# Optimization experiments

Measured on AMD Instinct MI355X. Metric: run time of the kernel, lower is better.

The kernel has to match this reference:

```python
import jax, jax.numpy as jnp
import numpy as np
from jax.ops import segment_sum

N = 100000
E = 3200000
IN_DIM = 128
HID = 64
L = 3
BN_EPS = 1e-5

def setup_inputs() -> dict:
    key = jax.random.key(0)
    ks = jax.random.split(key, 20)
    s = lambda k, *shape: jax.random.normal(k, shape, dtype=jnp.float32) * 0.05
    inp = {
        'x': jax.random.normal(ks[0], (N, IN_DIM), dtype=jnp.float32),
        'edge_index': jax.random.randint(ks[1], (2, E), 0, N, dtype=jnp.int32),
        'W_in': s(ks[2], IN_DIM, HID), 'b_in': jnp.zeros((HID,), jnp.float32),
        'W_gcn': s(ks[3], L, HID, HID), 'b_gcn': jnp.zeros((L, HID), jnp.float32),
        'bn_gamma': jnp.ones((L, HID), jnp.float32), 'bn_beta': jnp.zeros((L, HID), jnp.float32),
        'W_s1': s(ks[4], 3, HID // 2), 'b_s1': jnp.zeros((HID // 2,), jnp.float32),
        'W_s2': s(ks[5], HID // 2, HID), 'b_s2': jnp.zeros((HID,), jnp.float32),
        'W_o1': s(ks[6], 2 * HID, HID), 'b_o1': jnp.zeros((HID,), jnp.float32),
        'W_o2': s(ks[7], HID, HID // 2), 'b_o2': jnp.zeros((HID // 2,), jnp.float32),
        'W_o3': s(ks[8], HID // 2, 1), 'b_o3': jnp.zeros((1,), jnp.float32),
    }
    return inp

def _gcn_norm(row, col, n):
    # add self-loops, symmetric normalization (PyG GCNConv default)
    loop = jnp.arange(n, dtype=row.dtype)
    row_sl = jnp.concatenate([row, loop])
    col_sl = jnp.concatenate([col, loop])
    deg = segment_sum(jnp.ones_like(col_sl, jnp.float32), col_sl, num_segments=n)
    dis = jnp.where(deg > 0, jax.lax.rsqrt(jnp.maximum(deg, 1.0)), 0.0)
    norm = dis[row_sl] * dis[col_sl]
    return row_sl, col_sl, norm

def _structural(row, col, n):
    # vectorized equivalent of the O(N*E) python loops
    ones = jnp.ones(row.shape[0], jnp.float32)
    deg = segment_sum(ones, row, num_segments=n)          # out-degree over edge_index[0]
    dmax = deg.max()
    norm_deg = jnp.where(dmax > 0, deg / dmax, deg)
    infl_sum = segment_sum(deg[col], row, num_segments=n)  # sum of neighbor degrees
    infl = jnp.where(deg > 0, infl_sum / jnp.maximum(deg, 1.0), 0.0)
    imax = infl.max()
    infl = jnp.where(imax > 0, infl / imax, infl)
    clustering = jnp.zeros(n, jnp.float32)
    return jnp.stack([norm_deg, clustering, infl], axis=1)  # [N,3]

def reference(x, edge_index, W_in, b_in, W_gcn, b_gcn, bn_gamma, bn_beta,
              W_s1, b_s1, W_s2, b_s2, W_o1, b_o1, W_o2, b_o2, W_o3, b_o3):
    n = x.shape[0]
    row, col = edge_index[0], edge_index[1]
    h = x @ W_in + b_in
    row_sl, col_sl, norm = _gcn_norm(row, col, n)
    bn_scale = bn_gamma / jnp.sqrt(1.0 + BN_EPS)  # eval BN: running_mean=0, running_var=1
    for i in range(L):
        hw = h @ W_gcn[i]
        msg = hw[row_sl] * norm[:, None]              # [E+N, HID]
        h = segment_sum(msg, col_sl, num_segments=n) + b_gcn[i]
        h = h * bn_scale[i] + bn_beta[i]
        h = jax.nn.relu(h)
    sf = _structural(row, col, n)
    se = jax.nn.relu(sf @ W_s1 + b_s1) @ W_s2 + b_s2
    h = jnp.concatenate([h, se], axis=1)              # [N, 2*HID]
    h = jax.nn.relu(h @ W_o1 + b_o1)
    h = jax.nn.relu(h @ W_o2 + b_o2)
    return jax.nn.sigmoid(h @ W_o3 + b_o3)            # [N, 1]
```

## Files before the change

kernel.cpp:

```cpp
#include <hip/hip_runtime.h>
#include <hip/hip_bf16.h>
#include <hip/hip_fp16.h>

#define NBU8 65536
#define NB16 32768
#define TPBH 1024

__global__ void k_init(unsigned* __restrict__ maxima) {
    if (threadIdx.x < 2) maxima[threadIdx.x] = 0u;
}

__global__ __launch_bounds__(TPBH) void kh_hist(const int* __restrict__ keys,
                                                unsigned char* __restrict__ part,
                                                int E, int chunk, int npu) {
    __shared__ unsigned bins[NBU8 / 4];
    int b = blockIdx.x, t = threadIdx.x;
    int base = blockIdx.y * NBU8;
    int e0 = b * chunk, e1 = min(E, e0 + chunk);
    for (int j = t; j < NBU8 / 4; j += TPBH) bins[j] = 0u;
    __syncthreads();
    for (int e = e0 + t; e < e1; e += TPBH) {
        int k = keys[e] - base;
        if ((unsigned)k < NBU8) atomicAdd(&bins[k >> 2], 1u << ((k & 3) << 3));
    }
    __syncthreads();
    unsigned* dst = (unsigned*)(part + (size_t)b * npu + base);
    for (int j = t; j < NBU8 / 4; j += TPBH) dst[j] = bins[j];
}

__global__ __launch_bounds__(256) void k_scan1(const unsigned char* __restrict__ part,
                                               int nb, int npu,
                                               int* __restrict__ cnt,
                                               int* __restrict__ roff,
                                               int* __restrict__ bsum, int n) {
    __shared__ int s[256];
    int b = blockIdx.x, t = threadIdx.x;
    int i = b * 256 + t;
    int v = 0;
    if (i < n) {
        for (int k = 0; k < nb; ++k) v += part[(size_t)k * npu + i];
        cnt[i] = v;
    }
    s[t] = v;
    __syncthreads();
    for (int off = 1; off < 256; off <<= 1) {
        int x = (t >= off) ? s[t - off] : 0;
        __syncthreads();
        s[t] += x;
        __syncthreads();
    }
    if (i < n) roff[i] = s[t] - v;
    if (t == 255) bsum[b] = s[255];
}

__global__ __launch_bounds__(512) void k_scan2(int* __restrict__ bsum, int nb) {
    __shared__ int s[512];
    int t = threadIdx.x;
    int v = (t < nb) ? bsum[t] : 0;
    s[t] = v;
    __syncthreads();
    for (int off = 1; off < 512; off <<= 1) {
        int x = (t >= off) ? s[t - off] : 0;
        __syncthreads();
        s[t] += x;
        __syncthreads();
    }
    if (t < nb) bsum[t] = s[t] - v;
}

__global__ void k_scan3(int* __restrict__ roff, const int* __restrict__ bsum,
                        const int* __restrict__ cnt, float* __restrict__ dis, int n, int E) {
    int i = blockIdx.x * blockDim.x + threadIdx.x;
    if (i < n) {
        roff[i] += bsum[i >> 8];
        dis[i] = rsqrtf((float)cnt[i] + 1.0f);
    }
    if (i == 0) roff[n] = E;
}

__global__ void kh_prefix(unsigned char* __restrict__ part, int nb, int npu, int n) {
    int i = blockIdx.x * blockDim.x + threadIdx.x;
    if (i >= n) return;
    int run = 0;
    for (int g = 0; g < 8; ++g) {
        for (int b = g; b < nb; b += 8) {
            size_t idx = (size_t)b * npu + i;
            int v = part[idx];
            part[idx] = (unsigned char)run;
            run += v;
        }
    }
}

__global__ __launch_bounds__(TPBH) void kh_fill(const int* __restrict__ col,
                                                const int* __restrict__ row,
                                                const int* __restrict__ roff,
                                                const unsigned char* __restrict__ pref,
                                                int* __restrict__ esrc,
                                                int E, int chunk, int npu) {
    __shared__ unsigned curs[NBU8 / 4];
    int b = blockIdx.x, t = threadIdx.x;
    int base = blockIdx.y * NBU8;
    int e0 = b * chunk, e1 = min(E, e0 + chunk);
    for (int j = t; j < NBU8 / 4; j += TPBH) curs[j] = 0u;
    __syncthreads();
    const unsigned char* pb = pref + (size_t)b * npu;
    for (int e = e0 + t; e < e1; e += TPBH) {
        int c = col[e], r = row[e];
        int cl = c - base;
        if ((unsigned)cl < NBU8) {
            unsigned sh = (cl & 3) << 3;
            unsigned old = atomicAdd(&curs[cl >> 2], 1u << sh);
            unsigned local = (old >> sh) & 0xFFu;
            int slot = roff[c] + (int)pb[c] + (int)local;
            esrc[slot] = r;
        }
    }
}

__global__ __launch_bounds__(TPBH) void kh_histacc(const int* __restrict__ row,
                                                   const int* __restrict__ col,
                                                   const int* __restrict__ odeg_i,
                                                   unsigned short* __restrict__ part,
                                                   int E, int chunk, int npu) {
    __shared__ unsigned bins[NB16 / 2];
    int b = blockIdx.x, t = threadIdx.x;
    int base = blockIdx.y * NB16;
    int e0 = b * chunk, e1 = min(E, e0 + chunk);
    for (int j = t; j < NB16 / 2; j += TPBH) bins[j] = 0u;
    __syncthreads();
    for (int e = e0 + t; e < e1; e += TPBH) {
        int r = row[e] - base;
        if ((unsigned)r < NB16)
            atomicAdd(&bins[r >> 1], (unsigned)odeg_i[col[e]] << ((r & 1) << 4));
    }
    __syncthreads();
    unsigned* dst = (unsigned*)(part + (size_t)b * npu + base);
    for (int j = t; j < NB16 / 2; j += TPBH) dst[j] = bins[j];
}

__global__ void kh_reduce_odeg(const unsigned char* __restrict__ part,
                               float* __restrict__ odeg, int* __restrict__ odeg_i,
                               unsigned* __restrict__ maxima, int nb, int npu, int n) {
    int i = blockIdx.x * blockDim.x + threadIdx.x;
    float od = 0.f;
    if (i < n) {
        int s = 0;
        for (int b = 0; b < nb; ++b) s += part[(size_t)b * npu + i];
        od = (float)s;
        odeg[i] = od;
        odeg_i[i] = s;
    }
    for (int off = 32; off > 0; off >>= 1) od = fmaxf(od, __shfl_down(od, off));
    if ((threadIdx.x & 63) == 0) atomicMax(&maxima[0], __float_as_uint(od));
}

__global__ void kh_reduce_infl(const unsigned short* __restrict__ part,
                               const float* __restrict__ odeg,
                               float* __restrict__ infl, unsigned* __restrict__ maxima,
                               int nb, int npu, int n) {
    int i = blockIdx.x * blockDim.x + threadIdx.x;
    float fin = 0.f;
    if (i < n) {
        int s = 0;
        for (int b = 0; b < nb; ++b) s += part[(size_t)b * npu + i];
        float od = odeg[i];
        fin = (od > 0.f) ? (float)s / od : 0.f;
        infl[i] = fin;
    }
    for (int off = 32; off > 0; off >>= 1) fin = fmaxf(fin, __shfl_down(fin, off));
    if ((threadIdx.x & 63) == 0) atomicMax(&maxima[1], __float_as_uint(fin));
}

__global__ __launch_bounds__(256) void k_in_proj(const float* __restrict__ x,
                                                 const float* __restrict__ W,
                                                 const float* __restrict__ b,
                                                 float* __restrict__ h, int n) {
    __shared__ alignas(16) float Ws[128 * 64];
    __shared__ alignas(16) float xs[64 * 64];
    int t = threadIdx.x;
    int r0 = blockIdx.x * 64;
    for (int i = t; i < 128 * 64; i += 256) Ws[i] = W[i];

    int c = t & 63, rg = t >> 6;
    float acc[16];
    float bc = b[c];
#pragma unroll
    for (int i = 0; i < 16; ++i) acc[i] = bc;

    const float4* xs4 = (const float4*)xs;
    for (int half = 0; half < 2; ++half) {
        __syncthreads();
        for (int i = t; i < 64 * 16; i += 256) {
            int rr = i >> 4, k4 = i & 15;
            int r = r0 + rr;
            float4 v = (r < n) ? ((const float4*)x)[(size_t)r * 32 + half * 16 + k4]
                               : make_float4(0.f, 0.f, 0.f, 0.f);
            ((float4*)xs)[i] = v;
        }
        __syncthreads();
        for (int k4 = 0; k4 < 16; ++k4) {
            int kk = half * 64 + k4 * 4;
            float w0 = Ws[(kk + 0) * 64 + c];
            float w1 = Ws[(kk + 1) * 64 + c];
            float w2 = Ws[(kk + 2) * 64 + c];
            float w3 = Ws[(kk + 3) * 64 + c];
#pragma unroll
            for (int i = 0; i < 16; ++i) {
                float4 xv = xs4[(rg * 16 + i) * 16 + k4];
                acc[i] = fmaf(xv.x, w0, fmaf(xv.y, w1, fmaf(xv.z, w2, fmaf(xv.w, w3, acc[i]))));
            }
        }
    }
#pragma unroll
    for (int i = 0; i < 16; ++i) {
        int r = r0 + rg * 16 + i;
        if (r < n) h[(size_t)r * 64 + c] = acc[i];
    }
}

__global__ __launch_bounds__(256) void k_gcn_mm(const float* __restrict__ h,
                                                const float* __restrict__ Wg,
                                                const float* __restrict__ dis,
                                                unsigned* __restrict__ hws, int n) {
    __shared__ alignas(16) float Ws[64 * 64];
    __shared__ alignas(16) float xs[64 * 64];
    int t = threadIdx.x;
    int r0 = blockIdx.x * 64;
    for (int i = t; i < 64 * 64; i += 256) Ws[i] = Wg[i];
    for (int i = t; i < 64 * 16; i += 256) {
        int rr = i >> 4, k4 = i & 15;
        int r = r0 + rr;
        float4 v = (r < n) ? ((const float4*)h)[(size_t)r * 16 + k4]
                           : make_float4(0.f, 0.f, 0.f, 0.f);
        ((float4*)xs)[i] = v;
    }
    __syncthreads();
    int c2 = (t & 31) << 1, rg = t >> 5;
    const float4* xs4 = (const float4*)xs;
    float a0[8], a1[8];
#pragma unroll
    for (int i = 0; i < 8; ++i) { a0[i] = 0.f; a1[i] = 0.f; }
    for (int k4 = 0; k4 < 16; ++k4) {
        float wA0 = Ws[(k4 * 4 + 0) * 64 + c2],     wB0 = Ws[(k4 * 4 + 0) * 64 + c2 + 1];
        float wA1 = Ws[(k4 * 4 + 1) * 64 + c2],     wB1 = Ws[(k4 * 4 + 1) * 64 + c2 + 1];
        float wA2 = Ws[(k4 * 4 + 2) * 64 + c2],     wB2 = Ws[(k4 * 4 + 2) * 64 + c2 + 1];
        float wA3 = Ws[(k4 * 4 + 3) * 64 + c2],     wB3 = Ws[(k4 * 4 + 3) * 64 + c2 + 1];
#pragma unroll
        for (int i = 0; i < 8; ++i) {
            float4 xv = xs4[(rg * 8 + i) * 16 + k4];
            a0[i] = fmaf(xv.x, wA0, fmaf(xv.y, wA1, fmaf(xv.z, wA2, fmaf(xv.w, wA3, a0[i]))));
            a1[i] = fmaf(xv.x, wB0, fmaf(xv.y, wB1, fmaf(xv.z, wB2, fmaf(xv.w, wB3, a1[i]))));
        }
    }
#pragma unroll
    for (int i = 0; i < 8; ++i) {
        int r = r0 + rg * 8 + i;
        if (r < n) {
            float d = dis[r];
            __half2 hv = __floats2half2_rn(a0[i] * d, a1[i] * d);
            hws[(size_t)r * 32 + (t & 31)] = *(unsigned*)&hv;
        }
    }
}

__global__ __launch_bounds__(256) void k_gather(const int* __restrict__ roff,
                                                const int* __restrict__ esrc,
                                                const uint2* __restrict__ hws,
                                                const float* __restrict__ dis,
                                                const float* __restrict__ bg,
                                                const float* __restrict__ gamma,
                                                const float* __restrict__ beta,
                                                float* __restrict__ h, int n) {
    int t = threadIdx.x;
    int node = blockIdx.x * 16 + (t >> 4);
    int fl = t & 15;
    if (node >= n) return;

    int beg = roff[node], end = roff[node + 1];
    float acc0 = 0.f, acc1 = 0.f, acc2 = 0.f, acc3 = 0.f;
    union { unsigned u; __half2 h2; } cv;
#define ACC(a) { cv.u = (a).x; float2 f = __half22float2(cv.h2); acc0 += f.x; acc1 += f.y; \
                 cv.u = (a).y; f = __half22float2(cv.h2);        acc2 += f.x; acc3 += f.y; }
    {
        uint2 a = hws[(size_t)node * 16 + fl];
        ACC(a)
    }
    int e = beg;
    for (; e + 4 <= end; e += 4) {
        int r0 = esrc[e], r1 = esrc[e + 1], r2 = esrc[e + 2], r3 = esrc[e + 3];
        uint2 a = hws[(size_t)r0 * 16 + fl];
        uint2 b = hws[(size_t)r1 * 16 + fl];
        uint2 c = hws[(size_t)r2 * 16 + fl];
        uint2 d = hws[(size_t)r3 * 16 + fl];
        ACC(a) ACC(b) ACC(c) ACC(d)
    }
    for (; e < end; ++e) {
        uint2 a = hws[(size_t)esrc[e] * 16 + fl];
        ACC(a)
    }
#undef ACC
    float d = dis[node];
    float inv = rsqrtf(1.0f + 1e-5f);
    float4 g4 = ((const float4*)gamma)[fl];
    float4 b4 = ((const float4*)beta)[fl];
    float4 bg4 = ((const float4*)bg)[fl];
    float4 o;
    o.x = fmaxf(fmaf(acc0 * d + bg4.x, g4.x * inv, b4.x), 0.0f);
    o.y = fmaxf(fmaf(acc1 * d + bg4.y, g4.y * inv, b4.y), 0.0f);
    o.z = fmaxf(fmaf(acc2 * d + bg4.z, g4.z * inv, b4.z), 0.0f);
    o.w = fmaxf(fmaf(acc3 * d + bg4.w, g4.w * inv, b4.w), 0.0f);
    ((float4*)h)[(size_t)node * 16 + fl] = o;
}

__global__ __launch_bounds__(256) void k_final(const float* __restrict__ h,
                                               const float* __restrict__ odeg,
                                               const float* __restrict__ infl,
                                               const unsigned* __restrict__ maxima,
                                               const float* __restrict__ Ws1, const float* __restrict__ bs1,
                                               const float* __restrict__ Ws2, const float* __restrict__ bs2,
                                               const float* __restrict__ Wo1, const float* __restrict__ bo1,
                                               const float* __restrict__ Wo2, const float* __restrict__ bo2,
                                               const float* __restrict__ Wo3, const float* __restrict__ bo3,
                                               float* __restrict__ out, int n) {
    __shared__ alignas(16) float sWs1[96], sbs1[32], sWs2T[64 * 32], sbs2[64];
    __shared__ alignas(16) float sWo1[128 * 64], sbo1[64], sWo2[64 * 32], sbo2[32], sWo3[32];
    int t = threadIdx.x;
    for (int i = t; i < 96; i += 256) sWs1[i] = Ws1[i];
    for (int i = t; i < 2048; i += 256) {
        int j = i >> 6, k = i & 63;
        sWs2T[k * 32 + j] = Ws2[i];
    }
    for (int i = t; i < 8192; i += 256) sWo1[i] = Wo1[i];
    for (int i = t; i < 2048; i += 256) sWo2[i] = Wo2[i];
    if (t < 32) { sbs1[t] = bs1[t]; sbo2[t] = bo2[t]; sWo3[t] = Wo3[t]; }
    if (t < 64) { sbs2[t] = bs2[t]; sbo1[t] = bo1[t]; }
    __syncthreads();

    int i = blockIdx.x * 256 + t;
    if (i >= n) return;

    float dmax = __uint_as_float(maxima[0]);
    float imax = __uint_as_float(maxima[1]);
    float od = odeg[i];
    float sf0 = (dmax > 0.0f) ? od / dmax : od;
    float fin = infl[i];
    float sf2 = (imax > 0.0f) ? fin / imax : fin;

    float hid[32];
#pragma unroll
    for (int j = 0; j < 32; ++j)
        hid[j] = fmaxf(fmaf(sf0, sWs1[j], fmaf(sf2, sWs1[64 + j], sbs1[j])), 0.0f);

    float o1[64];
    const float4* sbo1_4 = (const float4*)sbo1;
#pragma unroll
    for (int c4 = 0; c4 < 16; ++c4) {
        float4 v = sbo1_4[c4];
        o1[c4 * 4] = v.x; o1[c4 * 4 + 1] = v.y; o1[c4 * 4 + 2] = v.z; o1[c4 * 4 + 3] = v.w;
    }

    const float4* sWo1_4 = (const float4*)sWo1;
    const float4* hrow = (const float4*)(h + (size_t)i * 64);
    for (int k4 = 0; k4 < 16; ++k4) {
        float4 hv = hrow[k4];
        float hv_[4] = {hv.x, hv.y, hv.z, hv.w};
#pragma unroll
        for (int j = 0; j < 4; ++j) {
            float hk = hv_[j];
            int k = k4 * 4 + j;
#pragma unroll
            for (int c4 = 0; c4 < 16; ++c4) {
                float4 w = sWo1_4[k * 16 + c4];
                o1[c4 * 4]     = fmaf(hk, w.x, o1[c4 * 4]);
                o1[c4 * 4 + 1] = fmaf(hk, w.y, o1[c4 * 4 + 1]);
                o1[c4 * 4 + 2] = fmaf(hk, w.z, o1[c4 * 4 + 2]);
                o1[c4 * 4 + 3] = fmaf(hk, w.w, o1[c4 * 4 + 3]);
            }
        }
    }
    const float4* sWs2T_4 = (const float4*)sWs2T;
    for (int k = 0; k < 64; ++k) {
        float sek = sbs2[k];
#pragma unroll
        for (int j4 = 0; j4 < 8; ++j4) {
            float4 w = sWs2T_4[k * 8 + j4];
            sek = fmaf(hid[j4 * 4], w.x, fmaf(hid[j4 * 4 + 1], w.y,
                  fmaf(hid[j4 * 4 + 2], w.z, fmaf(hid[j4 * 4 + 3], w.w, sek))));
        }
#pragma unroll
        for (int c4 = 0; c4 < 16; ++c4) {
            float4 w = sWo1_4[(64 + k) * 16 + c4];
            o1[c4 * 4]     = fmaf(sek, w.x, o1[c4 * 4]);
            o1[c4 * 4 + 1] = fmaf(sek, w.y, o1[c4 * 4 + 1]);
            o1[c4 * 4 + 2] = fmaf(sek, w.z, o1[c4 * 4 + 2]);
            o1[c4 * 4 + 3] = fmaf(sek, w.w, o1[c4 * 4 + 3]);
        }
    }

    float o2[32];
    const float4* sbo2_4 = (const float4*)sbo2;
#pragma unroll
    for (int c4 = 0; c4 < 8; ++c4) {
        float4 v = sbo2_4[c4];
        o2[c4 * 4] = v.x; o2[c4 * 4 + 1] = v.y; o2[c4 * 4 + 2] = v.z; o2[c4 * 4 + 3] = v.w;
    }
    const float4* sWo2_4 = (const float4*)sWo2;
#pragma unroll
    for (int c = 0; c < 64; ++c) {
        float v = fmaxf(o1[c], 0.0f);
#pragma unroll
        for (int c4 = 0; c4 < 8; ++c4) {
            float4 w = sWo2_4[c * 8 + c4];
            o2[c4 * 4]     = fmaf(v, w.x, o2[c4 * 4]);
            o2[c4 * 4 + 1] = fmaf(v, w.y, o2[c4 * 4 + 1]);
            o2[c4 * 4 + 2] = fmaf(v, w.z, o2[c4 * 4 + 2]);
            o2[c4 * 4 + 3] = fmaf(v, w.w, o2[c4 * 4 + 3]);
        }
    }

    float o3 = bo3[0];
#pragma unroll
    for (int c2 = 0; c2 < 32; ++c2)
        o3 = fmaf(fmaxf(o2[c2], 0.0f), sWo3[c2], o3);

    out[i] = 1.0f / (1.0f + __expf(-o3));
}

extern "C" void kernel_launch(void* const* d_in, const int* in_sizes, int n_in,
                              void* d_out, int out_size, void* d_ws, size_t ws_size,
                              hipStream_t stream) {
    const float* x     = (const float*)d_in[0];
    const int*   ei    = (const int*)d_in[1];
    const float* W_in  = (const float*)d_in[2];
    const float* b_in  = (const float*)d_in[3];
    const float* W_gcn = (const float*)d_in[4];
    const float* b_gcn = (const float*)d_in[5];
    const float* gamma = (const float*)d_in[6];
    const float* beta  = (const float*)d_in[7];
    const float* Ws1   = (const float*)d_in[8];
    const float* bs1   = (const float*)d_in[9];
    const float* Ws2   = (const float*)d_in[10];
    const float* bs2   = (const float*)d_in[11];
    const float* Wo1   = (const float*)d_in[12];
    const float* bo1   = (const float*)d_in[13];
    const float* Wo2   = (const float*)d_in[14];
    const float* bo2   = (const float*)d_in[15];
    const float* Wo3   = (const float*)d_in[16];
    const float* bo3   = (const float*)d_in[17];
    float* out = (float*)d_out;

    int n = in_sizes[0] / 128;
    int E = in_sizes[1] / 2;
    const int* row = ei;
    const int* col = ei + E;

    int npass8  = (n + NBU8 - 1) / NBU8;
    int npass16 = (n + NB16 - 1) / NB16;
    size_t NPU8  = (size_t)npass8 * NBU8;
    size_t NPU16 = (size_t)npass16 * NB16;

    auto al = [](size_t v) { return (v + 255) & ~(size_t)255; };
    size_t fixed = al((NPU8 + 256) * 4)
                 + al(NPU8 * 4)
                 + al(1024 * 4)
                 + 3 * al(NPU8 * 4)
                 + al(NPU8 * 4)
                 + al(256)
                 + al((size_t)E * 4)
                 + al((size_t)n * 64 * 4)
                 + al((size_t)n * 64 * 2);
    int NB = 128;
    auto partBytes = [&](int nb) {
        size_t a = (size_t)nb * NPU8, b2 = (size_t)nb * NPU16 * 2;
        return a > b2 ? a : b2;
    };
    while (NB > 32 && fixed + partBytes(NB) > ws_size) NB >>= 1;
    int chunk = (E + NB - 1) / NB;

    char* p = (char*)d_ws;
    unsigned char*  part8  = (unsigned char*)p;
    unsigned short* part16 = (unsigned short*)p;
    p += al(partBytes(NB));
    int* roff = (int*)p;        p += al((NPU8 + 256) * 4);
    int* cnt  = (int*)p;        p += al(NPU8 * 4);
    int* bsum = (int*)p;        p += al(1024 * 4);
    float* dis  = (float*)p;    p += al(NPU8 * 4);
    float* odeg = (float*)p;    p += al(NPU8 * 4);
    float* infl = (float*)p;    p += al(NPU8 * 4);
    int* odeg_i = (int*)p;      p += al(NPU8 * 4);
    unsigned* maxima = (unsigned*)p; p += al(256);
    int* esrc = (int*)p;        p += al((size_t)E * 4);
    float* h   = (float*)p;     p += al((size_t)n * 64 * 4);
    unsigned* hws = (unsigned*)p;

    int gn = (n + 255) / 256;

    k_init<<<1, 64, 0, stream>>>(maxima);

    kh_hist<<<dim3(NB, npass8), TPBH, 0, stream>>>(col, part8, E, chunk, (int)NPU8);
    k_scan1<<<gn, 256, 0, stream>>>(part8, NB, (int)NPU8, cnt, roff, bsum, n);
    k_scan2<<<1, 512, 0, stream>>>(bsum, gn);
    k_scan3<<<gn, 256, 0, stream>>>(roff, bsum, cnt, dis, n, E);
    kh_prefix<<<gn, 256, 0, stream>>>(part8, NB, (int)NPU8, n);
    kh_fill<<<dim3(NB, npass8), TPBH, 0, stream>>>(col, row, roff, part8, esrc, E, chunk, (int)NPU8);

    kh_hist<<<dim3(NB, npass8), TPBH, 0, stream>>>(row, part8, E, chunk, (int)NPU8);
    kh_reduce_odeg<<<gn, 256, 0, stream>>>(part8, odeg, odeg_i, maxima, NB, (int)NPU8, n);
    kh_histacc<<<dim3(NB, npass16), TPBH, 0, stream>>>(row, col, odeg_i, part16, E, chunk, (int)NPU16);
    kh_reduce_infl<<<gn, 256, 0, stream>>>(part16, odeg, infl, maxima, NB, (int)NPU16, n);

    k_in_proj<<<(n + 63) / 64, 256, 0, stream>>>(x, W_in, b_in, h, n);

    for (int l = 0; l < 3; ++l) {
        k_gcn_mm<<<(n + 63) / 64, 256, 0, stream>>>(h, W_gcn + (size_t)l * 64 * 64, dis, hws, n);
        k_gather<<<(n + 15) / 16, 256, 0, stream>>>(roff, esrc, (const uint2*)hws, dis,
                                                    b_gcn + l * 64, gamma + l * 64, beta + l * 64,
                                                    h, n);
    }

    k_final<<<gn, 256, 0, stream>>>(h, odeg, infl, maxima,
                                    Ws1, bs1, Ws2, bs2, Wo1, bo1, Wo2, bo2, Wo3, bo3,
                                    out, n);
}
```

Baseline: 799.7 us.

## Fuse GCN weight matmuls into gather and input projection, widen gather per node

Removes the separate k_gcn_mm kernels. The first layer's weight multiply moves into the input projection, and the next layer's multiply moves into each gather's epilogue using wavefront shuffles. Each gather now gives a full 64-lane wavefront to one node with four edge streams that are then reduced, instead of 16 lanes per node. It also folds the maxima init into the histogram kernel and doubles the histogram block count while halving the accumulation histogram's block count. This saves fp32 h round trips and kernel launches, at the cost of more shared memory per gather block and extra shuffles.

```diff
diff --git a/kernel.cpp b/kernel.cpp
--- a/kernel.cpp
+++ b/kernel.cpp
@@ -6,15 +6,13 @@
 #define NB16 32768
 #define TPBH 1024
 
-__global__ void k_init(unsigned* __restrict__ maxima) {
-    if (threadIdx.x < 2) maxima[threadIdx.x] = 0u;
-}
-
 __global__ __launch_bounds__(TPBH) void kh_hist(const int* __restrict__ keys,
                                                 unsigned char* __restrict__ part,
+                                                unsigned* __restrict__ maxima,
                                                 int E, int chunk, int npu) {
     __shared__ unsigned bins[NBU8 / 4];
     int b = blockIdx.x, t = threadIdx.x;
+    if (b == 0 && blockIdx.y == 0 && t < 2) maxima[t] = 0u;
     int base = blockIdx.y * NBU8;
     int e0 = b * chunk, e1 = min(E, e0 + chunk);
     for (int j = t; j < NBU8 / 4; j += TPBH) bins[j] = 0u;
@@ -175,12 +173,16 @@
 __global__ __launch_bounds__(256) void k_in_proj(const float* __restrict__ x,
                                                  const float* __restrict__ W,
                                                  const float* __restrict__ b,
-                                                 float* __restrict__ h, int n) {
+                                                 const float* __restrict__ Wg0,
+                                                 const float* __restrict__ dis,
+                                                 __half* __restrict__ hws, int n) {
     __shared__ alignas(16) float Ws[128 * 64];
     __shared__ alignas(16) float xs[64 * 64];
+    __shared__ alignas(16) float W2[64 * 64];
     int t = threadIdx.x;
     int r0 = blockIdx.x * 64;
     for (int i = t; i < 128 * 64; i += 256) Ws[i] = W[i];
+    for (int i = t; i < 64 * 64; i += 256) W2[i] = Wg0[i];
 
     int c = t & 63, rg = t >> 6;
     float acc[16];
@@ -212,105 +214,97 @@
             }
         }
     }
-#pragma unroll
+    __syncthreads();
+#pragma unroll
+    for (int i = 0; i < 16; ++i) xs[(rg * 16 + i) * 64 + c] = acc[i];
+    __syncthreads();
+#pragma unroll 2
     for (int i = 0; i < 16; ++i) {
         int r = r0 + rg * 16 + i;
-        if (r < n) h[(size_t)r * 64 + c] = acc[i];
-    }
-}
-
-__global__ __launch_bounds__(256) void k_gcn_mm(const float* __restrict__ h,
-                                                const float* __restrict__ Wg,
-                                                const float* __restrict__ dis,
-                                                unsigned* __restrict__ hws, int n) {
-    __shared__ alignas(16) float Ws[64 * 64];
-    __shared__ alignas(16) float xs[64 * 64];
-    int t = threadIdx.x;
-    int r0 = blockIdx.x * 64;
-    for (int i = t; i < 64 * 64; i += 256) Ws[i] = Wg[i];
-    for (int i = t; i < 64 * 16; i += 256) {
-        int rr = i >> 4, k4 = i & 15;
-        int r = r0 + rr;
-        float4 v = (r < n) ? ((const float4*)h)[(size_t)r * 16 + k4]
-                           : make_float4(0.f, 0.f, 0.f, 0.f);
-        ((float4*)xs)[i] = v;
-    }
-    __syncthreads();
-    int c2 = (t & 31) << 1, rg = t >> 5;
-    const float4* xs4 = (const float4*)xs;
-    float a0[8], a1[8];
-#pragma unroll
-    for (int i = 0; i < 8; ++i) { a0[i] = 0.f; a1[i] = 0.f; }
-    for (int k4 = 0; k4 < 16; ++k4) {
-        float wA0 = Ws[(k4 * 4 + 0) * 64 + c2],     wB0 = Ws[(k4 * 4 + 0) * 64 + c2 + 1];
-        float wA1 = Ws[(k4 * 4 + 1) * 64 + c2],     wB1 = Ws[(k4 * 4 + 1) * 64 + c2 + 1];
-        float wA2 = Ws[(k4 * 4 + 2) * 64 + c2],     wB2 = Ws[(k4 * 4 + 2) * 64 + c2 + 1];
-        float wA3 = Ws[(k4 * 4 + 3) * 64 + c2],     wB3 = Ws[(k4 * 4 + 3) * 64 + c2 + 1];
-#pragma unroll
-        for (int i = 0; i < 8; ++i) {
-            float4 xv = xs4[(rg * 8 + i) * 16 + k4];
-            a0[i] = fmaf(xv.x, wA0, fmaf(xv.y, wA1, fmaf(xv.z, wA2, fmaf(xv.w, wA3, a0[i]))));
-            a1[i] = fmaf(xv.x, wB0, fmaf(xv.y, wB1, fmaf(xv.z, wB2, fmaf(xv.w, wB3, a1[i]))));
-        }
-    }
-#pragma unroll
-    for (int i = 0; i < 8; ++i) {
-        int r = r0 + rg * 8 + i;
-        if (r < n) {
-            float d = dis[r];
-            __half2 hv = __floats2half2_rn(a0[i] * d, a1[i] * d);
-            hws[(size_t)r * 32 + (t & 31)] = *(unsigned*)&hv;
-        }
-    }
-}
-
-__global__ __launch_bounds__(256) void k_gather(const int* __restrict__ roff,
+        if (r >= n) break;
+        float s = 0.f;
+#pragma unroll
+        for (int k4 = 0; k4 < 16; ++k4) {
+            float4 hv = xs4[(rg * 16 + i) * 16 + k4];
+            s = fmaf(hv.x, W2[(k4 * 4 + 0) * 64 + c],
+                fmaf(hv.y, W2[(k4 * 4 + 1) * 64 + c],
+                fmaf(hv.z, W2[(k4 * 4 + 2) * 64 + c],
+                fmaf(hv.w, W2[(k4 * 4 + 3) * 64 + c], s))));
+        }
+        hws[(size_t)r * 64 + c] = __float2half(s * dis[r]);
+    }
+}
+
+template<int FUSE_MM>
+__global__ __launch_bounds__(512) void k_gather(const int* __restrict__ roff,
                                                 const int* __restrict__ esrc,
-                                                const uint2* __restrict__ hws,
+                                                const uint2* __restrict__ hws_in,
                                                 const float* __restrict__ dis,
                                                 const float* __restrict__ bg,
                                                 const float* __restrict__ gamma,
                                                 const float* __restrict__ beta,
-                                                float* __restrict__ h, int n) {
+                                                const float* __restrict__ Wg,
+                                                __half* __restrict__ hws_out,
+                                                float* __restrict__ hout, int n) {
+    __shared__ alignas(16) float sW[FUSE_MM ? 64 * 64 : 64];
     int t = threadIdx.x;
-    int node = blockIdx.x * 16 + (t >> 4);
-    int fl = t & 15;
+    if (FUSE_MM) {
+        for (int i = t; i < 64 * 64; i += 512) sW[i] = Wg[i];
+        __syncthreads();
+    }
+    int wid = t >> 6, lane = t & 63;
+    int node = blockIdx.x * 8 + wid;
     if (node >= n) return;
+    int grp = lane >> 4, fl = lane & 15;
 
     int beg = roff[node], end = roff[node + 1];
-    float acc0 = 0.f, acc1 = 0.f, acc2 = 0.f, acc3 = 0.f;
+    float a0 = 0.f, a1 = 0.f, a2 = 0.f, a3 = 0.f;
     union { unsigned u; __half2 h2; } cv;
-#define ACC(a) { cv.u = (a).x; float2 f = __half22float2(cv.h2); acc0 += f.x; acc1 += f.y; \
-                 cv.u = (a).y; f = __half22float2(cv.h2);        acc2 += f.x; acc3 += f.y; }
-    {
-        uint2 a = hws[(size_t)node * 16 + fl];
-        ACC(a)
-    }
-    int e = beg;
-    for (; e + 4 <= end; e += 4) {
-        int r0 = esrc[e], r1 = esrc[e + 1], r2 = esrc[e + 2], r3 = esrc[e + 3];
-        uint2 a = hws[(size_t)r0 * 16 + fl];
-        uint2 b = hws[(size_t)r1 * 16 + fl];
-        uint2 c = hws[(size_t)r2 * 16 + fl];
-        uint2 d = hws[(size_t)r3 * 16 + fl];
-        ACC(a) ACC(b) ACC(c) ACC(d)
-    }
-    for (; e < end; ++e) {
-        uint2 a = hws[(size_t)esrc[e] * 16 + fl];
-        ACC(a)
-    }
+#define ACC(v) { cv.u = (v).x; float2 f_ = __half22float2(cv.h2); a0 += f_.x; a1 += f_.y; \
+                 cv.u = (v).y; f_ = __half22float2(cv.h2);        a2 += f_.x; a3 += f_.y; }
+    if (grp == 0) { uint2 v = hws_in[(size_t)node * 16 + fl]; ACC(v) }
+    int e = beg + grp;
+    for (; e + 4 < end; e += 8) {
+        int r0 = esrc[e], r1 = esrc[e + 4];
+        uint2 v0 = hws_in[(size_t)r0 * 16 + fl];
+        uint2 v1 = hws_in[(size_t)r1 * 16 + fl];
+        ACC(v0) ACC(v1)
+    }
+    if (e < end) { uint2 v = hws_in[(size_t)esrc[e] * 16 + fl]; ACC(v) }
 #undef ACC
+    a0 += __shfl_xor(a0, 16); a1 += __shfl_xor(a1, 16);
+    a2 += __shfl_xor(a2, 16); a3 += __shfl_xor(a3, 16);
+    a0 += __shfl_xor(a0, 32); a1 += __shfl_xor(a1, 32);
+    a2 += __shfl_xor(a2, 32); a3 += __shfl_xor(a3, 32);
+
     float d = dis[node];
     float inv = rsqrtf(1.0f + 1e-5f);
     float4 g4 = ((const float4*)gamma)[fl];
     float4 b4 = ((const float4*)beta)[fl];
     float4 bg4 = ((const float4*)bg)[fl];
     float4 o;
-    o.x = fmaxf(fmaf(acc0 * d + bg4.x, g4.x * inv, b4.x), 0.0f);
-    o.y = fmaxf(fmaf(acc1 * d + bg4.y, g4.y * inv, b4.y), 0.0f);
-    o.z = fmaxf(fmaf(acc2 * d + bg4.z, g4.z * inv, b4.z), 0.0f);
-    o.w = fmaxf(fmaf(acc3 * d + bg4.w, g4.w * inv, b4.w), 0.0f);
-    ((float4*)h)[(size_t)node * 16 + fl] = o;
+    o.x = fmaxf(fmaf(a0 * d + bg4.x, g4.x * inv, b4.x), 0.0f);
+    o.y = fmaxf(fmaf(a1 * d + bg4.y, g4.y * inv, b4.y), 0.0f);
+    o.z = fmaxf(fmaf(a2 * d + bg4.z, g4.z * inv, b4.z), 0.0f);
+    o.w = fmaxf(fmaf(a3 * d + bg4.w, g4.w * inv, b4.w), 0.0f);
+
+    if (FUSE_MM) {
+        float s = 0.f;
+#pragma unroll
+        for (int q = 0; q < 16; ++q) {
+            float h0 = __shfl(o.x, q);
+            float h1 = __shfl(o.y, q);
+            float h2 = __shfl(o.z, q);
+            float h3 = __shfl(o.w, q);
+            s = fmaf(h0, sW[(q * 4 + 0) * 64 + lane],
+                fmaf(h1, sW[(q * 4 + 1) * 64 + lane],
+                fmaf(h2, sW[(q * 4 + 2) * 64 + lane],
+                fmaf(h3, sW[(q * 4 + 3) * 64 + lane], s))));
+        }
+        hws_out[(size_t)node * 64 + lane] = __float2half(s * d);
+    } else {
+        if (grp == 0) ((float4*)hout)[(size_t)node * 16 + fl] = o;
+    }
 }
 
 __global__ __launch_bounds__(256) void k_final(const float* __restrict__ h,
@@ -469,14 +463,17 @@
                  + al(256)
                  + al((size_t)E * 4)
                  + al((size_t)n * 64 * 4)
-                 + al((size_t)n * 64 * 2);
-    int NB = 128;
+                 + 2 * al((size_t)n * 64 * 2);
+    int NB = 256;
     auto partBytes = [&](int nb) {
-        size_t a = (size_t)nb * NPU8, b2 = (size_t)nb * NPU16 * 2;
+        size_t a = (size_t)nb * NPU8;
+        size_t b2 = (size_t)(nb / 2) * NPU16 * 2;
         return a > b2 ? a : b2;
     };
     while (NB > 32 && fixed + partBytes(NB) > ws_size) NB >>= 1;
-    int chunk = (E + NB - 1) / NB;
+    int NBa = NB / 2;
+    int chunk  = (E + NB - 1) / NB;
+    int chunkA = (E + NBa - 1) / NBa;
 
     char* p = (char*)d_ws;
     unsigned char*  part8  = (unsigned char*)p;
@@ -492,32 +489,35 @@
     unsigned* maxima = (unsigned*)p; p += al(256);
     int* esrc = (int*)p;        p += al((size_t)E * 4);
     float* h   = (float*)p;     p += al((size_t)n * 64 * 4);
-    unsigned* hws = (unsigned*)p;
+    __half* hwsA = (__half*)p;  p += al((size_t)n * 64 * 2);
+    __half* hwsB = (__half*)p;
 
     int gn = (n + 255) / 256;
 
-    k_init<<<1, 64, 0, stream>>>(maxima);
-
-    kh_hist<<<dim3(NB, npass8), TPBH, 0, stream>>>(col, part8, E, chunk, (int)NPU8);
+    kh_hist<<<dim3(NB, npass8), TPBH, 0, stream>>>(col, part8, maxima, E, chunk, (int)NPU8);
     k_scan1<<<gn, 256, 0, stream>>>(part8, NB, (int)NPU8, cnt, roff, bsum, n);
     k_scan2<<<1, 512, 0, stream>>>(bsum, gn);
     k_scan3<<<gn, 256, 0, stream>>>(roff, bsum, cnt, dis, n, E);
     kh_prefix<<<gn, 256, 0, stream>>>(part8, NB, (int)NPU8, n);
     kh_fill<<<dim3(NB, npass8), TPBH, 0, stream>>>(col, row, roff, part8, esrc, E, chunk, (int)NPU8);
 
-    kh_hist<<<dim3(NB, npass8), TPBH, 0, stream>>>(row, part8, E, chunk, (int)NPU8);
+    kh_hist<<<dim3(NB, npass8), TPBH, 0, stream>>>(row, part8, maxima, E, chunk, (int)NPU8);
     kh_reduce_odeg<<<gn, 256, 0, stream>>>(part8, odeg, odeg_i, maxima, NB, (int)NPU8, n);
-    kh_histacc<<<dim3(NB, npass16), TPBH, 0, stream>>>(row, col, odeg_i, part16, E, chunk, (int)NPU16);
-    kh_reduce_infl<<<gn, 256, 0, stream>>>(part16, odeg, infl, maxima, NB, (int)NPU16, n);
-
-    k_in_proj<<<(n + 63) / 64, 256, 0, stream>>>(x, W_in, b_in, h, n);
-
-    for (int l = 0; l < 3; ++l) {
-        k_gcn_mm<<<(n + 63) / 64, 256, 0, stream>>>(h, W_gcn + (size_t)l * 64 * 64, dis, hws, n);
-        k_gather<<<(n + 15) / 16, 256, 0, stream>>>(roff, esrc, (const uint2*)hws, dis,
-                                                    b_gcn + l * 64, gamma + l * 64, beta + l * 64,
-                                                    h, n);
-    }
+    kh_histacc<<<dim3(NBa, npass16), TPBH, 0, stream>>>(row, col, odeg_i, part16, E, chunkA, (int)NPU16);
+    kh_reduce_infl<<<gn, 256, 0, stream>>>(part16, odeg, infl, maxima, NBa, (int)NPU16, n);
+
+    k_in_proj<<<(n + 63) / 64, 256, 0, stream>>>(x, W_in, b_in, W_gcn, dis, hwsA, n);
+
+    int gg = (n + 7) / 8;
+    k_gather<1><<<gg, 512, 0, stream>>>(roff, esrc, (const uint2*)hwsA, dis,
+                                        b_gcn + 0 * 64, gamma + 0 * 64, beta + 0 * 64,
+                                        W_gcn + (size_t)1 * 64 * 64, hwsB, nullptr, n);
+    k_gather<1><<<gg, 512, 0, stream>>>(roff, esrc, (const uint2*)hwsB, dis,
+                                        b_gcn + 1 * 64, gamma + 1 * 64, beta + 1 * 64,
+                                        W_gcn + (size_t)2 * 64 * 64, hwsA, nullptr, n);
+    k_gather<0><<<gg, 512, 0, stream>>>(roff, esrc, (const uint2*)hwsA, dis,
+                                        b_gcn + 2 * 64, gamma + 2 * 64, beta + 2 * 64,
+                                        nullptr, nullptr, h, n);
 
     k_final<<<gn, 256, 0, stream>>>(h, odeg, infl, maxima,
                                     Ws1, bs1, Ws2, bs2, Wo1, bo1, Wo2, bo2, Wo3, bo3,
```

Measured after the change: 1.001 ms. 1.25x slower.
